# Kernel optimization log

Measured on AMD Instinct MI355X. Metric: run time of the kernel, lower is better.

## Reference

```python
import jax, jax.numpy as jnp
import numpy as np
from jax import lax

K = 3       # kernel_size
STRIDE = 1
PAD = 1
DIL = 1


def setup_inputs() -> dict:
    key = jax.random.key(0)
    ks = jax.random.split(key, 4)
    B, Cin, Cout, H, W = 4, 128, 256, 64, 64
    x = jax.random.normal(ks[0], (B, Cin, H, W), jnp.float32)
    # offset/mask conv params: out channels = 3*K*K (groups=1). Small weights
    # keep predicted offsets within a few pixels (module inits them to zero).
    om_w = jax.random.normal(ks[1], (3 * K * K, Cin, K, K), jnp.float32) * 0.01
    om_b = jnp.zeros((3 * K * K,), jnp.float32)
    weight = jax.random.normal(ks[2], (Cout, Cin, K, K), jnp.float32) * (1.0 / np.sqrt(Cin * K * K))
    bias = jnp.zeros((Cout,), jnp.float32)
    return {"x": x, "om_w": om_w, "om_b": om_b, "weight": weight, "bias": bias}


def _deform_conv(x, om_w, om_b, weight, bias):
    B, Cin, H, W = x.shape
    Cout = weight.shape[0]
    kk = K * K

    # offset/mask conv (stride/pad/dilation same as main conv)
    om = lax.conv_general_dilated(
        x, om_w, (STRIDE, STRIDE), [(PAD, PAD), (PAD, PAD)],
        rhs_dilation=(DIL, DIL), dimension_numbers=('NCHW', 'OIHW', 'NCHW'))
    om = om + om_b[None, :, None, None]
    Ho, Wo = om.shape[2], om.shape[3]

    off = om[:, :2 * kk].reshape(B, 2, kk, Ho, Wo)
    off_x, off_y = off[:, 0], off[:, 1]           # [B,kk,Ho,Wo]
    mask = jax.nn.sigmoid(om[:, 2 * kk:])          # [B,kk,Ho,Wo]

    # base grid (output pixel -> input pixel of kernel center)
    gy, gx = jnp.meshgrid(jnp.arange(Ho, dtype=x.dtype), jnp.arange(Wo, dtype=x.dtype), indexing='ij')
    base_x = gx * STRIDE - PAD
    base_y = gy * STRIDE - PAD
    # kernel taps centered at 0: arange(-(K-1)//2, (K+1)//2)
    r = jnp.arange(-(K - 1) // 2, (K + 1) // 2, dtype=x.dtype)
    koy, kox = jnp.meshgrid(r * DIL, r * DIL, indexing='ij')
    kox = kox.reshape(kk, 1, 1)
    koy = koy.reshape(kk, 1, 1)

    sx = base_x[None, None] + kox[None] + off_x    # [B,kk,Ho,Wo]
    sy = base_y[None, None] + koy[None] + off_y

    # Faithful to original: coords normalized with align_corners=True formula
    # (2*s/(size-1)-1) but grid_sample called with align_corners=False, i.e.
    # pixel coord = ((g+1)*size - 1)/2  =>  s*size/(size-1) - 0.5
    ix = sx * (W / (W - 1.0)) - 0.5
    iy = sy * (H / (H - 1.0)) - 0.5

    x0 = jnp.floor(ix)
    y0 = jnp.floor(iy)
    x1 = x0 + 1.0
    y1 = y0 + 1.0
    wx1 = ix - x0
    wx0 = 1.0 - wx1
    wy1 = iy - y0
    wy0 = 1.0 - wy1

    img = x.reshape(B, Cin, H * W)

    def gather(yy, xx):
        yi = yy.astype(jnp.int32)
        xi = xx.astype(jnp.int32)
        valid = ((yi >= 0) & (yi < H) & (xi >= 0) & (xi < W)).astype(x.dtype)
        idx = jnp.clip(yi, 0, H - 1) * W + jnp.clip(xi, 0, W - 1)   # [B,kk,Ho,Wo]
        v = jax.vmap(lambda im, i: im[:, i])(img, idx.reshape(B, -1))  # [B,Cin,kk*Ho*Wo]
        return v.reshape(B, Cin, kk, Ho, Wo) * valid[:, None]

    # bilinear (zeros padding) sample at kk taps per output pixel
    sampled = (gather(y0, x0) * (wy0 * wx0)[:, None]
               + gather(y0, x1) * (wy0 * wx1)[:, None]
               + gather(y1, x0) * (wy1 * wx0)[:, None]
               + gather(y1, x1) * (wy1 * wx1)[:, None])   # [B,Cin,kk,Ho,Wo]

    sampled = sampled * mask[:, None]
    w = weight.reshape(Cout, Cin, kk)
    out = jnp.einsum('bckhw,ock->bohw', sampled, w)
    return out + bias[None, :, None, None]


def reference(x, om_w, om_b, weight, bias):
    return _deform_conv(x, om_w, om_b, weight, bias)
```

## Files before the change

### kernel.cpp

```cpp
#include <hip/hip_runtime.h>
#include <hip/hip_bf16.h>

typedef _Float16 h4 __attribute__((ext_vector_type(4)));
typedef _Float16 h8 __attribute__((ext_vector_type(8)));
typedef float f32x4 __attribute__((ext_vector_type(4)));

#define CIN 128
#define COUT 256
#define KDIM (CIN*9)

__global__ void k_prep(const float* __restrict__ wgt, const float* __restrict__ om_w,
                       unsigned short* __restrict__ Wf, unsigned short* __restrict__ omWf) {
    int bid = blockIdx.x;
    if (bid < 1152) {
        int f = bid * 256 + threadIdx.x;
        int e = f & 7, l = (f >> 3) & 63, of = (f >> 9) & 15, kch = f >> 13;
        int o = of * 16 + (l & 15);
        int kc = kch * 32 + (l >> 4) * 8 + e;
        int k = kc >> 7, c = kc & 127;
        _Float16 hv = (_Float16)wgt[(size_t)o * KDIM + c * 9 + k];
        Wf[f] = *(unsigned short*)&hv;
    } else {
        int f = (bid - 1152) * 256 + threadIdx.x;
        int e = f & 7, l = (f >> 3) & 63, of = (f >> 9) & 1, kch = f >> 10;
        int o = of * 16 + (l & 15);
        int c = (kch & 3) * 32 + (l >> 4) * 8 + e;
        int k = kch >> 2;
        float v = (o < 27) ? om_w[(size_t)o * KDIM + c * 9 + k] : 0.f;
        _Float16 hv = (_Float16)v;
        omWf[f] = *(unsigned short*)&hv;
    }
}

__global__ __launch_bounds__(256) void k_transpose(const float* __restrict__ x,
                                                   unsigned short* __restrict__ xT) {
    __shared__ unsigned short tile[64][132];
    const int b = blockIdx.x >> 6, y = blockIdx.x & 63;
    const float* xp = x + (size_t)b * CIN * 4096 + y * 64;
    const int w = threadIdx.x & 63, cg = threadIdx.x >> 6;
#pragma unroll
    for (int cc = 0; cc < CIN; cc += 4) {
        int c = cc + cg;
        _Float16 hv = (_Float16)xp[(size_t)c * 4096 + w];
        tile[w][c] = *(unsigned short*)&hv;
    }
    __syncthreads();
    unsigned short* orow = xT + (size_t)(b * 4096 + y * 64) * CIN;
#pragma unroll
    for (int i = 0; i < 8; ++i) {
        int j = threadIdx.x + i * 256;
        int w2 = j >> 5, c2 = (j & 31) * 4;
        ushort4 v = *(ushort4*)&tile[w2][c2];
        ((ushort4*)orow)[j] = v;
    }
}

__global__ __launch_bounds__(512) void k_fused(const unsigned short* __restrict__ xT_u,
                                               const unsigned short* __restrict__ omWf_u,
                                               const float* __restrict__ om_b,
                                               const unsigned short* __restrict__ Wf_u,
                                               const float* __restrict__ bias,
                                               float* __restrict__ out) {
    const int b = blockIdx.x >> 6, h = blockIdx.x & 63;
    const int tid = threadIdx.x;
    const int wv = tid >> 6, lane = tid & 63;
    const int khalf = lane >> 4, lr = lane & 15;

    __shared__ int   s_off[4][576];
    __shared__ float s_wt[4][576];
    __shared__ h8    s_tile[2][64 * 8];
    __shared__ float red[2][64][28];

    const _Float16* xb = (const _Float16*)xT_u + (size_t)b * (4096 * CIN);

    {
        const h8* Af = (const h8*)omWf_u;
        const int pg = wv & 3, kh2 = wv >> 2;
        const int p = pg * 16 + lr;
        const int k0 = kh2 ? 5 : 0, k1 = kh2 ? 9 : 5;
        f32x4 acc0 = (f32x4){0.f, 0.f, 0.f, 0.f};
        f32x4 acc1 = (f32x4){0.f, 0.f, 0.f, 0.f};
        for (int k = k0; k < k1; ++k) {
            const int ky = k / 3, kx = k - ky * 3;
            const int y = h + ky - 1, xq = p + kx - 1;
            const bool valid = ((unsigned)y < 64u) && ((unsigned)xq < 64u);
            const _Float16* src = xb + ((y * 64 + xq) * CIN);
#pragma unroll
            for (int cg = 0; cg < 4; ++cg) {
                h8 bf = {};
                if (valid) bf = *(const h8*)(src + cg * 32 + khalf * 8);
                const int kch = k * 4 + cg;
                h8 a0 = Af[(kch * 2 + 0) * 64 + lane];
                h8 a1 = Af[(kch * 2 + 1) * 64 + lane];
                acc0 = __builtin_amdgcn_mfma_f32_16x16x32_f16(a0, bf, acc0, 0, 0, 0);
                acc1 = __builtin_amdgcn_mfma_f32_16x16x32_f16(a1, bf, acc1, 0, 0, 0);
            }
        }
#pragma unroll
        for (int r = 0; r < 4; ++r) {
            red[kh2][p][khalf * 4 + r] = acc0[r];
            int row1 = 16 + khalf * 4 + r;
            if (row1 < 27) red[kh2][p][row1] = acc1[r];
        }
    }
    __syncthreads();

    for (int e = tid; e < 576; e += 512) {
        int k = e >> 6, p = e & 63;
        float offx = red[0][p][k]      + red[1][p][k]      + om_b[k];
        float offy = red[0][p][9 + k]  + red[1][p][9 + k]  + om_b[9 + k];
        float mv   = red[0][p][18 + k] + red[1][p][18 + k] + om_b[18 + k];
        float mask = 1.f / (1.f + __expf(-mv));
        int ky = k / 3, kx = k - ky * 3;
        const float SC = 64.f / 63.f;
        float ix = ((float)(p + kx - 2) + offx) * SC - 0.5f;
        float iy = ((float)(h + ky - 2) + offy) * SC - 0.5f;
        float fx0 = floorf(ix), fy0 = floorf(iy);
        float wx1 = ix - fx0, wx0 = 1.f - wx1;
        float wy1 = iy - fy0, wy0 = 1.f - wy1;
        int x0 = (int)fx0, y0 = (int)fy0;
        int x1 = x0 + 1, y1 = y0 + 1;
        bool vx0 = (unsigned)x0 < 64u, vx1 = (unsigned)x1 < 64u;
        bool vy0 = (unsigned)y0 < 64u, vy1 = (unsigned)y1 < 64u;
        int xc0 = min(max(x0, 0), 63), xc1 = min(max(x1, 0), 63);
        int yc0 = min(max(y0, 0), 63), yc1 = min(max(y1, 0), 63);
        s_off[0][e] = (yc0 * 64 + xc0) * CIN;
        s_off[1][e] = (yc0 * 64 + xc1) * CIN;
        s_off[2][e] = (yc1 * 64 + xc0) * CIN;
        s_off[3][e] = (yc1 * 64 + xc1) * CIN;
        s_wt[0][e] = (vy0 && vx0) ? wy0 * wx0 * mask : 0.f;
        s_wt[1][e] = (vy0 && vx1) ? wy0 * wx1 * mask : 0.f;
        s_wt[2][e] = (vy1 && vx0) ? wy1 * wx0 * mask : 0.f;
        s_wt[3][e] = (vy1 && vx1) ? wy1 * wx1 * mask : 0.f;
    }
    __syncthreads();

    const int p  = tid >> 3;
    const int ci = tid & 7;
    const h8* Wf8 = (const h8*)Wf_u;
    const int wslot = ci ^ (p & 7);

    f32x4 acc[2][4];
#pragma unroll
    for (int i = 0; i < 2; ++i)
#pragma unroll
        for (int j = 0; j < 4; ++j) acc[i][j] = (f32x4){0.f, 0.f, 0.f, 0.f};

    {
        const int e0 = p;
        const int cb = ci * 8;
        h8 v00 = *(const h8*)(xb + s_off[0][e0] + cb);
        h8 v01 = *(const h8*)(xb + s_off[1][e0] + cb);
        h8 v10 = *(const h8*)(xb + s_off[2][e0] + cb);
        h8 v11 = *(const h8*)(xb + s_off[3][e0] + cb);
        const float m00 = s_wt[0][e0], m01 = s_wt[1][e0], m10 = s_wt[2][e0], m11 = s_wt[3][e0];
        h8 pk;
#pragma unroll
        for (int j = 0; j < 8; ++j) {
            float r = m00 * (float)v00[j] + m01 * (float)v01[j]
                    + m10 * (float)v10[j] + m11 * (float)v11[j];
            pk[j] = (_Float16)r;
        }
        s_tile[0][p * 8 + wslot] = pk;
    }
    __syncthreads();

    for (int ch = 0; ch < 18; ++ch) {
        const int cur = ch & 1;
        const int nxt = ch + 1;

        h8 v00, v01, v10, v11;
        float m00, m01, m10, m11;
        if (nxt < 18) {
            const int kn = nxt >> 1;
            const int e = kn * 64 + p;
            const int cb = (nxt & 1) * 64 + ci * 8;
            v00 = *(const h8*)(xb + s_off[0][e] + cb);
            v01 = *(const h8*)(xb + s_off[1][e] + cb);
            v10 = *(const h8*)(xb + s_off[2][e] + cb);
            v11 = *(const h8*)(xb + s_off[3][e] + cb);
            m00 = s_wt[0][e]; m01 = s_wt[1][e]; m10 = s_wt[2][e]; m11 = s_wt[3][e];
        }

        const int k = ch >> 1, chalf = ch & 1;
#pragma unroll
        for (int ks = 0; ks < 2; ++ks) {
            const int kch = k * 4 + chalf * 2 + ks;
            h8 a0 = Wf8[(kch * 16 + wv * 2 + 0) * 64 + lane];
            h8 a1 = Wf8[(kch * 16 + wv * 2 + 1) * 64 + lane];
#pragma unroll
            for (int pf = 0; pf < 4; ++pf) {
                const int row = pf * 16 + lr;
                h8 bf = s_tile[cur][row * 8 + ((ks * 4 + khalf) ^ (row & 7))];
                acc[0][pf] = __builtin_amdgcn_mfma_f32_16x16x32_f16(a0, bf, acc[0][pf], 0, 0, 0);
                acc[1][pf] = __builtin_amdgcn_mfma_f32_16x16x32_f16(a1, bf, acc[1][pf], 0, 0, 0);
            }
        }

        if (nxt < 18) {
            h8 pk;
#pragma unroll
            for (int j = 0; j < 8; ++j) {
                float r = m00 * (float)v00[j] + m01 * (float)v01[j]
                        + m10 * (float)v10[j] + m11 * (float)v11[j];
                pk[j] = (_Float16)r;
            }
            s_tile[cur ^ 1][p * 8 + wslot] = pk;
        }
        __syncthreads();
    }

    float* outb = out + (size_t)b * COUT * 4096 + h * 64;
#pragma unroll
    for (int i = 0; i < 2; ++i) {
#pragma unroll
        for (int r = 0; r < 4; ++r) {
            const int o = wv * 32 + i * 16 + khalf * 4 + r;
            const float bo = bias[o];
            float* orow = outb + (size_t)o * 4096;
#pragma unroll
            for (int pf = 0; pf < 4; ++pf)
                orow[pf * 16 + lr] = acc[i][pf][r] + bo;
        }
    }
}

extern "C" void kernel_launch(void* const* d_in, const int* in_sizes, int n_in,
                              void* d_out, int out_size, void* d_ws, size_t ws_size,
                              hipStream_t stream) {
    const float* x    = (const float*)d_in[0];
    const float* om_w = (const float*)d_in[1];
    const float* om_b = (const float*)d_in[2];
    const float* wgt  = (const float*)d_in[3];
    const float* bias = (const float*)d_in[4];
    float* out = (float*)d_out;

    char* ws = (char*)d_ws;
    unsigned short* xT   = (unsigned short*)ws;
    unsigned short* Wf   = (unsigned short*)(ws + 4194304);
    unsigned short* omWf = (unsigned short*)(ws + 4194304 + 589824);

    k_prep     <<<1296, 256, 0, stream>>>(wgt, om_w, Wf, omWf);
    k_transpose<<<256, 256, 0, stream>>>(x, xT);
    k_fused    <<<256, 512, 0, stream>>>(xT, omWf, om_b, Wf, bias, out);
}
```

Measured before the change: 47.77 us.

## Merge prep and transpose kernels; split fused kernel into half-row blocks

Result: faster. 44.48 us (-6.9%).

```diff
diff --git a/kernel.cpp b/kernel.cpp
--- a/kernel.cpp
+++ b/kernel.cpp
@@ -9,11 +9,35 @@
 #define COUT 256
 #define KDIM (CIN*9)
 
-__global__ void k_prep(const float* __restrict__ wgt, const float* __restrict__ om_w,
-                       unsigned short* __restrict__ Wf, unsigned short* __restrict__ omWf) {
-    int bid = blockIdx.x;
-    if (bid < 1152) {
-        int f = bid * 256 + threadIdx.x;
+__global__ __launch_bounds__(256) void k_pt(const float* __restrict__ x,
+                                            const float* __restrict__ wgt,
+                                            const float* __restrict__ om_w,
+                                            unsigned short* __restrict__ xT,
+                                            unsigned short* __restrict__ Wf,
+                                            unsigned short* __restrict__ omWf) {
+    __shared__ unsigned short tile[64][132];
+    const int bid = blockIdx.x;
+    if (bid < 256) {
+        const int b = bid >> 6, y = bid & 63;
+        const float* xp = x + (size_t)b * CIN * 4096 + y * 64;
+        const int w = threadIdx.x & 63, cg = threadIdx.x >> 6;
+#pragma unroll
+        for (int cc = 0; cc < CIN; cc += 4) {
+            int c = cc + cg;
+            _Float16 hv = (_Float16)xp[(size_t)c * 4096 + w];
+            tile[w][c] = *(unsigned short*)&hv;
+        }
+        __syncthreads();
+        unsigned short* orow = xT + (size_t)(b * 4096 + y * 64) * CIN;
+#pragma unroll
+        for (int i = 0; i < 8; ++i) {
+            int j = threadIdx.x + i * 256;
+            int w2 = j >> 5, c2 = (j & 31) * 4;
+            ushort4 v = *(ushort4*)&tile[w2][c2];
+            ((ushort4*)orow)[j] = v;
+        }
+    } else if (bid < 1408) {
+        int f = (bid - 256) * 256 + threadIdx.x;
         int e = f & 7, l = (f >> 3) & 63, of = (f >> 9) & 15, kch = f >> 13;
         int o = of * 16 + (l & 15);
         int kc = kch * 32 + (l >> 4) * 8 + e;
@@ -21,7 +45,7 @@
         _Float16 hv = (_Float16)wgt[(size_t)o * KDIM + c * 9 + k];
         Wf[f] = *(unsigned short*)&hv;
     } else {
-        int f = (bid - 1152) * 256 + threadIdx.x;
+        int f = (bid - 1408) * 256 + threadIdx.x;
         int e = f & 7, l = (f >> 3) & 63, of = (f >> 9) & 1, kch = f >> 10;
         int o = of * 16 + (l & 15);
         int c = (kch & 3) * 32 + (l >> 4) * 8 + e;
@@ -32,51 +56,31 @@
     }
 }
 
-__global__ __launch_bounds__(256) void k_transpose(const float* __restrict__ x,
-                                                   unsigned short* __restrict__ xT) {
-    __shared__ unsigned short tile[64][132];
-    const int b = blockIdx.x >> 6, y = blockIdx.x & 63;
-    const float* xp = x + (size_t)b * CIN * 4096 + y * 64;
-    const int w = threadIdx.x & 63, cg = threadIdx.x >> 6;
-#pragma unroll
-    for (int cc = 0; cc < CIN; cc += 4) {
-        int c = cc + cg;
-        _Float16 hv = (_Float16)xp[(size_t)c * 4096 + w];
-        tile[w][c] = *(unsigned short*)&hv;
-    }
-    __syncthreads();
-    unsigned short* orow = xT + (size_t)(b * 4096 + y * 64) * CIN;
-#pragma unroll
-    for (int i = 0; i < 8; ++i) {
-        int j = threadIdx.x + i * 256;
-        int w2 = j >> 5, c2 = (j & 31) * 4;
-        ushort4 v = *(ushort4*)&tile[w2][c2];
-        ((ushort4*)orow)[j] = v;
-    }
-}
-
-__global__ __launch_bounds__(512) void k_fused(const unsigned short* __restrict__ xT_u,
-                                               const unsigned short* __restrict__ omWf_u,
-                                               const float* __restrict__ om_b,
-                                               const unsigned short* __restrict__ Wf_u,
-                                               const float* __restrict__ bias,
-                                               float* __restrict__ out) {
-    const int b = blockIdx.x >> 6, h = blockIdx.x & 63;
+__global__ __launch_bounds__(256, 3) void k_fused(const unsigned short* __restrict__ xT_u,
+                                                  const unsigned short* __restrict__ omWf_u,
+                                                  const float* __restrict__ om_b,
+                                                  const unsigned short* __restrict__ Wf_u,
+                                                  const float* __restrict__ bias,
+                                                  float* __restrict__ out) {
+    const int bid = blockIdx.x;
+    const int half = bid & 1, h = (bid >> 1) & 63, b = bid >> 7;
+    const int p_base = half * 32;
     const int tid = threadIdx.x;
     const int wv = tid >> 6, lane = tid & 63;
     const int khalf = lane >> 4, lr = lane & 15;
 
-    __shared__ int   s_off[4][576];
-    __shared__ float s_wt[4][576];
-    __shared__ h8    s_tile[2][64 * 8];
-    __shared__ float red[2][64][28];
+    __shared__ int   s_off[4][288];
+    __shared__ float s_wt[4][288];
+    __shared__ h8    s_tile[2][32 * 8];
+    __shared__ float red[2][32][28];
 
     const _Float16* xb = (const _Float16*)xT_u + (size_t)b * (4096 * CIN);
 
     {
         const h8* Af = (const h8*)omWf_u;
-        const int pg = wv & 3, kh2 = wv >> 2;
-        const int p = pg * 16 + lr;
+        const int pg = wv & 1, kh2 = wv >> 1;
+        const int pl = pg * 16 + lr;
+        const int p = p_base + pl;
         const int k0 = kh2 ? 5 : 0, k1 = kh2 ? 9 : 5;
         f32x4 acc0 = (f32x4){0.f, 0.f, 0.f, 0.f};
         f32x4 acc1 = (f32x4){0.f, 0.f, 0.f, 0.f};
@@ -98,18 +102,19 @@
         }
 #pragma unroll
         for (int r = 0; r < 4; ++r) {
-            red[kh2][p][khalf * 4 + r] = acc0[r];
+            red[kh2][pl][khalf * 4 + r] = acc0[r];
             int row1 = 16 + khalf * 4 + r;
-            if (row1 < 27) red[kh2][p][row1] = acc1[r];
+            if (row1 < 27) red[kh2][pl][row1] = acc1[r];
         }
     }
     __syncthreads();
 
-    for (int e = tid; e < 576; e += 512) {
-        int k = e >> 6, p = e & 63;
-        float offx = red[0][p][k]      + red[1][p][k]      + om_b[k];
-        float offy = red[0][p][9 + k]  + red[1][p][9 + k]  + om_b[9 + k];
-        float mv   = red[0][p][18 + k] + red[1][p][18 + k] + om_b[18 + k];
+    for (int e = tid; e < 288; e += 256) {
+        int k = e >> 5, pl = e & 31;
+        int p = p_base + pl;
+        float offx = red[0][pl][k]      + red[1][pl][k]      + om_b[k];
+        float offy = red[0][pl][9 + k]  + red[1][pl][9 + k]  + om_b[9 + k];
+        float mv   = red[0][pl][18 + k] + red[1][pl][18 + k] + om_b[18 + k];
         float mask = 1.f / (1.f + __expf(-mv));
         int ky = k / 3, kx = k - ky * 3;
         const float SC = 64.f / 63.f;
@@ -140,11 +145,11 @@
     const h8* Wf8 = (const h8*)Wf_u;
     const int wslot = ci ^ (p & 7);
 
-    f32x4 acc[2][4];
-#pragma unroll
-    for (int i = 0; i < 2; ++i)
-#pragma unroll
-        for (int j = 0; j < 4; ++j) acc[i][j] = (f32x4){0.f, 0.f, 0.f, 0.f};
+    f32x4 acc[4][2];
+#pragma unroll
+    for (int i = 0; i < 4; ++i)
+#pragma unroll
+        for (int j = 0; j < 2; ++j) acc[i][j] = (f32x4){0.f, 0.f, 0.f, 0.f};
 
     {
         const int e0 = p;
@@ -173,7 +178,7 @@
         float m00, m01, m10, m11;
         if (nxt < 18) {
             const int kn = nxt >> 1;
-            const int e = kn * 64 + p;
+            const int e = kn * 32 + p;
             const int cb = (nxt & 1) * 64 + ci * 8;
             v00 = *(const h8*)(xb + s_off[0][e] + cb);
             v01 = *(const h8*)(xb + s_off[1][e] + cb);
@@ -186,15 +191,21 @@
 #pragma unroll
         for (int ks = 0; ks < 2; ++ks) {
             const int kch = k * 4 + chalf * 2 + ks;
-            h8 a0 = Wf8[(kch * 16 + wv * 2 + 0) * 64 + lane];
-            h8 a1 = Wf8[(kch * 16 + wv * 2 + 1) * 64 + lane];
-#pragma unroll
-            for (int pf = 0; pf < 4; ++pf) {
+            h8 a[4];
+#pragma unroll
+            for (int i = 0; i < 4; ++i)
+                a[i] = Wf8[(kch * 16 + wv * 4 + i) * 64 + lane];
+            h8 bf[2];
+#pragma unroll
+            for (int pf = 0; pf < 2; ++pf) {
                 const int row = pf * 16 + lr;
-                h8 bf = s_tile[cur][row * 8 + ((ks * 4 + khalf) ^ (row & 7))];
-                acc[0][pf] = __builtin_amdgcn_mfma_f32_16x16x32_f16(a0, bf, acc[0][pf], 0, 0, 0);
-                acc[1][pf] = __builtin_amdgcn_mfma_f32_16x16x32_f16(a1, bf, acc[1][pf], 0, 0, 0);
+                bf[pf] = s_tile[cur][row * 8 + ((ks * 4 + khalf) ^ (row & 7))];
             }
+#pragma unroll
+            for (int i = 0; i < 4; ++i)
+#pragma unroll
+                for (int pf = 0; pf < 2; ++pf)
+                    acc[i][pf] = __builtin_amdgcn_mfma_f32_16x16x32_f16(a[i], bf[pf], acc[i][pf], 0, 0, 0);
         }
 
         if (nxt < 18) {
@@ -210,16 +221,16 @@
         __syncthreads();
     }
 
-    float* outb = out + (size_t)b * COUT * 4096 + h * 64;
-#pragma unroll
-    for (int i = 0; i < 2; ++i) {
+    float* outb = out + (size_t)b * COUT * 4096 + h * 64 + p_base;
+#pragma unroll
+    for (int i = 0; i < 4; ++i) {
 #pragma unroll
         for (int r = 0; r < 4; ++r) {
-            const int o = wv * 32 + i * 16 + khalf * 4 + r;
+            const int o = wv * 64 + i * 16 + khalf * 4 + r;
             const float bo = bias[o];
             float* orow = outb + (size_t)o * 4096;
 #pragma unroll
-            for (int pf = 0; pf < 4; ++pf)
+            for (int pf = 0; pf < 2; ++pf)
                 orow[pf * 16 + lr] = acc[i][pf][r] + bo;
         }
     }
@@ -240,7 +251,6 @@
     unsigned short* Wf   = (unsigned short*)(ws + 4194304);
     unsigned short* omWf = (unsigned short*)(ws + 4194304 + 589824);
 
-    k_prep     <<<1296, 256, 0, stream>>>(wgt, om_w, Wf, omWf);
-    k_transpose<<<256, 256, 0, stream>>>(x, xT);
-    k_fused    <<<256, 512, 0, stream>>>(xT, omWf, om_b, Wf, bias, out);
+    k_pt   <<<1552, 256, 0, stream>>>(x, wgt, om_w, xT, Wf, omWf);
+    k_fused<<<512, 256, 0, stream>>>(xT, omWf, om_b, Wf, bias, out);
 }
```
